# Optimization experiments

Hardware: AMD Instinct MI355X
Metric: run time of the kernel (lower is better)

The kernel has to match this reference:

```python
import jax, jax.numpy as jnp
import numpy as np

HEADS = 8

def setup_inputs() -> dict:
    key = jax.random.key(0)
    k1, k2 = jax.random.split(key)
    f_s = jax.random.normal(k1, (8, 256, 32, 32), dtype=jnp.float32)
    f_t = jax.random.normal(k2, (8, 256, 32, 32), dtype=jnp.float32)
    return {"f_s": f_s, "f_t": f_t}

def _to_tokens(x, heads):
    # 'b (h d) x y -> b h (x y) d'
    b, c, h, w = x.shape
    d = c // heads
    return x.reshape(b, heads, d, h * w).transpose(0, 1, 3, 2)

def reference(f_s, f_t):
    b, c, h, w = f_s.shape
    q = _to_tokens(f_s, HEADS)   # [b, H, n, d]
    k = _to_tokens(f_t, HEADS)
    v = _to_tokens(f_s, HEADS)
    # unscaled QK^T softmax V (faithful to source: no 1/sqrt(d) scaling)
    sim = jnp.einsum('bhid,bhjd->bhij', q, k)          # [b, H, n, n]
    attn = jax.nn.softmax(sim, axis=-1)
    out = jnp.einsum('bhij,bhjd->bhid', attn, v)       # [b, H, n, d]
    # 'b h (x y) d -> b (h d) x y'
    out = out.transpose(0, 1, 3, 2).reshape(b, c, h, w)
    loss = jnp.mean((out - f_t) ** 2)
    return loss
```

## Files before the change

kernel.cpp:

```cpp
#include <hip/hip_runtime.h>
#include <hip/hip_bf16.h>


typedef __attribute__((ext_vector_type(4))) float f32x4;
typedef __attribute__((ext_vector_type(8))) short bf16x8;
typedef __attribute__((ext_vector_type(4))) unsigned u32x4;

#define QOFF 0
#define KOFF 16384
#define VOFF 24576
#define ROFF 32768

__device__ __forceinline__ unsigned cvtpk(float a, float b) {
    unsigned r;
    asm("v_cvt_pk_bf16_f32 %0, %1, %2" : "=v"(r) : "v"(a), "v"(b));
    return r;
}
#define SWAP32(a, b) asm("v_permlane32_swap_b32 %0, %1" : "+v"(a), "+v"(b))
#define SWAP16(a, b) asm("v_permlane16_swap_b32 %0, %1" : "+v"(a), "+v"(b))

__device__ __forceinline__ float exp2fast(float x) {
#if __has_builtin(__builtin_amdgcn_exp2f)
    return __builtin_amdgcn_exp2f(x);
#else
    return exp2f(x);
#endif
}

__global__ __launch_bounds__(512, 2)
void attn_mse_kernel(const float* __restrict__ fs, const float* __restrict__ ft,
                     float* __restrict__ out)
{
    __shared__ __align__(16) unsigned char smem[32832];

    const int tid  = threadIdx.x;
    const int lane = tid & 63;
    const int w    = tid >> 6;
    const int g    = lane >> 4;
    const int c    = lane & 15;

    const int bid  = blockIdx.x;
    const int x    = bid & 7, y = bid >> 3;
    const int pair = x * 8 + (y & 7);
    const int q0   = (y >> 3) * 256;

    const float* qb = fs + (size_t)pair * 32768;
    const float* kb = ft + (size_t)pair * 32768;

    {
        unsigned* lq = (unsigned*)(smem + QOFF) + w * 512;
        #pragma unroll
        for (int is = 0; is < 2; ++is) {
            const int row0 = q0 + w * 32 + is * 16;
            #pragma unroll
            for (int p = 0; p < 4; ++p) {
                const int dp = 4 * p + g;
                const float* src = qb + (size_t)(2 * dp) * 1024 + row0 + c;
                lq[is * 256 + p * 64 + c * 4 + g] =
                    cvtpk(src[0] * 1.44269504f, src[1024] * 1.44269504f);
            }
        }
    }
    const bf16x8 qf0 = *(const bf16x8*)(smem + QOFF + w * 2048 + lane * 16);
    const bf16x8 qf1 = *(const bf16x8*)(smem + QOFF + w * 2048 + 1024 + lane * 16);

    const int s_k = w >> 1, h_k = w & 1;
    float  kr[4];
    float4 vr;
    const int d_v = w * 4 + g;

    auto LOADK = [&](int t) {
        const int row0 = t * 64 + s_k * 16;
        #pragma unroll
        for (int pp = 0; pp < 2; ++pp) {
            const int dp = 4 * (2 * h_k + pp) + g;
            const float* src = kb + (size_t)(2 * dp) * 1024 + row0 + c;
            kr[2 * pp] = src[0]; kr[2 * pp + 1] = src[1024];
        }
    };
    auto LOADV = [&](int t) {
        vr = *(const float4*)(qb + (size_t)d_v * 1024 + t * 64 + 4 * c);
    };
    auto STORE = [&](int buf) {
        unsigned* lk = (unsigned*)(smem + KOFF + buf * 4096) + s_k * 256;
        #pragma unroll
        for (int pp = 0; pp < 2; ++pp) {
            const int p = 2 * h_k + pp;
            lk[p * 64 + c * 4 + g] = cvtpk(kr[2 * pp], kr[2 * pp + 1]);
        }
        unsigned char* lv = smem + VOFF + buf * 4096;
        const unsigned lo = cvtpk(vr.x, vr.y), hi = cvtpk(vr.z, vr.w);
        *(unsigned long long*)(lv + d_v * 128 + ((8 * c) ^ ((d_v & 7) << 4))) =
            (unsigned long long)lo | ((unsigned long long)hi << 32);
    };

    LOADK(0); LOADV(0);
    STORE(0);

    f32x4 O[2][2];
    #pragma unroll
    for (int a = 0; a < 2; ++a)
        #pragma unroll
        for (int b = 0; b < 2; ++b)
            O[a][b] = f32x4{0.f, 0.f, 0.f, 0.f};
    float l0 = 0.f, l1 = 0.f;

    int cur = 0;
    for (int t = 0; t < 16; ++t) {
        if (t < 15) { LOADK(t + 1); LOADV(t + 1); }
        __syncthreads();
        const unsigned char* bK = smem + KOFF + cur * 4096;
        const unsigned char* bV = smem + VOFF + cur * 4096;

        bf16x8 kf[4], vb[2][2];
        #pragma unroll
        for (int Mt = 0; Mt < 4; ++Mt)
            kf[Mt] = *(const bf16x8*)(bK + Mt * 1024 + lane * 16);
        #pragma unroll
        for (int ks = 0; ks < 2; ++ks)
            #pragma unroll
            for (int df = 0; df < 2; ++df)
                vb[ks][df] = *(const bf16x8*)(bV + (c + 16 * df) * 128 +
                               (((unsigned)(ks * 64 + g * 16)) ^ ((c & 7) << 4)));

        f32x4 S[4][2];
        #pragma unroll
        for (int Mt = 0; Mt < 4; ++Mt) {
            const f32x4 z = {0.f, 0.f, 0.f, 0.f};
            S[Mt][0] = __builtin_amdgcn_mfma_f32_16x16x32_bf16(kf[Mt], qf0, z, 0, 0, 0);
            S[Mt][1] = __builtin_amdgcn_mfma_f32_16x16x32_bf16(kf[Mt], qf1, z, 0, 0, 0);
        }

        float ps0 = 0.f, ps1 = 0.f;
        #pragma unroll
        for (int Mt = 0; Mt < 4; ++Mt)
            #pragma unroll
            for (int r = 0; r < 4; ++r) {
                const float p0 = exp2fast(S[Mt][0][r]);
                const float p1 = exp2fast(S[Mt][1][r]);
                S[Mt][0][r] = p0; ps0 += p0;
                S[Mt][1][r] = p1; ps1 += p1;
            }
        l0 += ps0; l1 += ps1;

        #pragma unroll
        for (int is = 0; is < 2; ++is) {
            #pragma unroll
            for (int ks = 0; ks < 2; ++ks) {
                unsigned u0 = cvtpk(S[2 * ks][is][0],     S[2 * ks][is][1]);
                unsigned u1 = cvtpk(S[2 * ks][is][2],     S[2 * ks][is][3]);
                unsigned u2 = cvtpk(S[2 * ks + 1][is][0], S[2 * ks + 1][is][1]);
                unsigned u3 = cvtpk(S[2 * ks + 1][is][2], S[2 * ks + 1][is][3]);
                SWAP32(u0, u2); SWAP32(u1, u3);
                SWAP16(u0, u2); SWAP16(u1, u3);
                const u32x4 pw = {u0, u1, u2, u3};
                const bf16x8 pa = __builtin_bit_cast(bf16x8, pw);
                O[is][0] = __builtin_amdgcn_mfma_f32_16x16x32_bf16(pa, vb[ks][0], O[is][0], 0, 0, 0);
                O[is][1] = __builtin_amdgcn_mfma_f32_16x16x32_bf16(pa, vb[ks][1], O[is][1], 0, 0, 0);
            }
        }

        if (t < 15) STORE(cur ^ 1);
        cur ^= 1;
    }

    l0 += __shfl_xor(l0, 16); l0 += __shfl_xor(l0, 32);
    l1 += __shfl_xor(l1, 16); l1 += __shfl_xor(l1, 32);
    const float li0 = 1.0f / l0;
    const float li1 = 1.0f / l1;

    float acc = 0.f;
    const int n0 = q0 + w * 32;
    #pragma unroll
    for (int is = 0; is < 2; ++is) {
        const float liv = is ? li1 : li0;
        #pragma unroll
        for (int r = 0; r < 4; ++r) {
            const float lr = __shfl(liv, g * 4 + r);
            const int n = n0 + is * 16 + g * 4 + r;
            #pragma unroll
            for (int Nd = 0; Nd < 2; ++Nd) {
                const int d = Nd * 16 + c;
                const float oo = O[is][Nd][r] * lr;
                const float tv = kb[(size_t)d * 1024 + n];
                const float e = oo - tv;
                acc += e * e;
            }
        }
    }
    #pragma unroll
    for (int off = 1; off < 64; off <<= 1) acc += __shfl_xor(acc, off);
    float* lred = (float*)(smem + ROFF);
    if (lane == 0) lred[w] = acc;
    __syncthreads();
    if (tid == 0) {
        float s = 0.f;
        #pragma unroll
        for (int i = 0; i < 8; ++i) s += lred[i];
        atomicAdd(out, s * (1.0f / 2097152.0f));
    }
}

extern "C" void kernel_launch(void* const* d_in, const int* in_sizes, int n_in,
                              void* d_out, int out_size, void* d_ws, size_t ws_size,
                              hipStream_t stream) {
    const float* fs = (const float*)d_in[0];
    const float* ft = (const float*)d_in[1];
    float* out = (float*)d_out;
    hipMemsetAsync(out, 0, sizeof(float), stream);
    attn_mse_kernel<<<dim3(256), dim3(512), 0, stream>>>(fs, ft, out);
}
```

Baseline: 28.46 us.

## Stage full K/V into 128KB LDS upfront, drop per-tile syncs, stagger tile order

Replaces the double-buffered K/V streaming loop with a single upfront load of all 16 K and V tiles into 128KB of shared memory, so the main loop has no barriers. Global loads become float4-vectorised with an XOR-swizzled LDS layout for the K and Q fragments, and each wave starts at a different tile offset to spread LDS bank traffic. MFMA sections are wrapped in s_setprio to favour matrix issue. The cost is losing overlap between global loads and compute, and with 128KB LDS per block only one block fits per CU, which defeats the launch bound of two blocks.

```diff
diff --git a/kernel.cpp b/kernel.cpp
--- a/kernel.cpp
+++ b/kernel.cpp
@@ -6,10 +6,8 @@
 typedef __attribute__((ext_vector_type(8))) short bf16x8;
 typedef __attribute__((ext_vector_type(4))) unsigned u32x4;
 
-#define QOFF 0
-#define KOFF 16384
-#define VOFF 24576
-#define ROFF 32768
+#define KOFF 0
+#define VOFF 65536
 
 __device__ __forceinline__ unsigned cvtpk(float a, float b) {
     unsigned r;
@@ -31,7 +29,7 @@
 void attn_mse_kernel(const float* __restrict__ fs, const float* __restrict__ ft,
                      float* __restrict__ out)
 {
-    __shared__ __align__(16) unsigned char smem[32832];
+    __shared__ __align__(16) unsigned char smem[131072];
 
     const int tid  = threadIdx.x;
     const int lane = tid & 63;
@@ -40,62 +38,60 @@
     const int c    = lane & 15;
 
     const int bid  = blockIdx.x;
-    const int x    = bid & 7, y = bid >> 3;
-    const int pair = x * 8 + (y & 7);
-    const int q0   = (y >> 3) * 256;
+    const int pair = (bid & 7) * 8 + ((bid >> 3) & 7);
+    const int q0   = (bid >> 6) * 256;
 
     const float* qb = fs + (size_t)pair * 32768;
     const float* kb = ft + (size_t)pair * 32768;
 
+    const int p_ = c >> 2, jq = c & 3;
+    const int dp = 4 * p_ + g;
+    const int w0 = p_ * 64 + 16 * jq + 4 * (0 ^ p_) + g;
+    const int w1 = p_ * 64 + 16 * jq + 4 * (1 ^ p_) + g;
+    const int w2 = p_ * 64 + 16 * jq + 4 * (2 ^ p_) + g;
+    const int w3 = p_ * 64 + 16 * jq + 4 * (3 ^ p_) + g;
+
     {
-        unsigned* lq = (unsigned*)(smem + QOFF) + w * 512;
-        #pragma unroll
-        for (int is = 0; is < 2; ++is) {
-            const int row0 = q0 + w * 32 + is * 16;
-            #pragma unroll
-            for (int p = 0; p < 4; ++p) {
-                const int dp = 4 * p + g;
-                const float* src = qb + (size_t)(2 * dp) * 1024 + row0 + c;
-                lq[is * 256 + p * 64 + c * 4 + g] =
-                    cvtpk(src[0] * 1.44269504f, src[1024] * 1.44269504f);
-            }
-        }
-    }
-    const bf16x8 qf0 = *(const bf16x8*)(smem + QOFF + w * 2048 + lane * 16);
-    const bf16x8 qf1 = *(const bf16x8*)(smem + QOFF + w * 2048 + 1024 + lane * 16);
-
-    const int s_k = w >> 1, h_k = w & 1;
-    float  kr[4];
-    float4 vr;
-    const int d_v = w * 4 + g;
-
-    auto LOADK = [&](int t) {
-        const int row0 = t * 64 + s_k * 16;
-        #pragma unroll
-        for (int pp = 0; pp < 2; ++pp) {
-            const int dp = 4 * (2 * h_k + pp) + g;
-            const float* src = kb + (size_t)(2 * dp) * 1024 + row0 + c;
-            kr[2 * pp] = src[0]; kr[2 * pp + 1] = src[1024];
-        }
-    };
-    auto LOADV = [&](int t) {
-        vr = *(const float4*)(qb + (size_t)d_v * 1024 + t * 64 + 4 * c);
-    };
-    auto STORE = [&](int buf) {
-        unsigned* lk = (unsigned*)(smem + KOFF + buf * 4096) + s_k * 256;
-        #pragma unroll
-        for (int pp = 0; pp < 2; ++pp) {
-            const int p = 2 * h_k + pp;
-            lk[p * 64 + c * 4 + g] = cvtpk(kr[2 * pp], kr[2 * pp + 1]);
-        }
-        unsigned char* lv = smem + VOFF + buf * 4096;
-        const unsigned lo = cvtpk(vr.x, vr.y), hi = cvtpk(vr.z, vr.w);
-        *(unsigned long long*)(lv + d_v * 128 + ((8 * c) ^ ((d_v & 7) << 4))) =
-            (unsigned long long)lo | ((unsigned long long)hi << 32);
-    };
-
-    LOADK(0); LOADV(0);
-    STORE(0);
+        const float sc = 1.44269504f;
+        #pragma unroll
+        for (int st = 0; st < 2; ++st) {
+            const float* r0 = qb + (size_t)(2 * dp) * 1024 + (q0 + w * 32 + st * 16) + 4 * jq;
+            const float4 a = *(const float4*)(r0);
+            const float4 b = *(const float4*)(r0 + 1024);
+            unsigned* dst = (unsigned*)(smem + VOFF + w * 2048 + st * 1024);
+            dst[w0] = cvtpk(a.x * sc, b.x * sc);
+            dst[w1] = cvtpk(a.y * sc, b.y * sc);
+            dst[w2] = cvtpk(a.z * sc, b.z * sc);
+            dst[w3] = cvtpk(a.w * sc, b.w * sc);
+        }
+    }
+    const bf16x8 qf0 = *(const bf16x8*)(smem + VOFF + w * 2048 + ((lane ^ g) << 4));
+    const bf16x8 qf1 = *(const bf16x8*)(smem + VOFF + w * 2048 + 1024 + ((lane ^ g) << 4));
+    __syncthreads();
+
+    #pragma unroll
+    for (int st = 0; st < 8; ++st) {
+        const float* r0 = kb + (size_t)(2 * dp) * 1024 + (w * 128 + st * 16) + 4 * jq;
+        const float4 a = *(const float4*)(r0);
+        const float4 b = *(const float4*)(r0 + 1024);
+        unsigned* dst = (unsigned*)(smem + KOFF + (w * 8 + st) * 1024);
+        dst[w0] = cvtpk(a.x, b.x);
+        dst[w1] = cvtpk(a.y, b.y);
+        dst[w2] = cvtpk(a.z, b.z);
+        dst[w3] = cvtpk(a.w, b.w);
+    }
+    {
+        const int dv = w * 4 + g;
+        #pragma unroll
+        for (int tt = 0; tt < 16; ++tt) {
+            const float4 vv = *(const float4*)(qb + (size_t)dv * 1024 + tt * 64 + 4 * c);
+            const unsigned lo = cvtpk(vv.x, vv.y), hi = cvtpk(vv.z, vv.w);
+            *(unsigned long long*)(smem + VOFF + tt * 4096 + dv * 128 +
+                                   ((8 * c) ^ ((dv & 7) << 4))) =
+                (unsigned long long)lo | ((unsigned long long)hi << 32);
+        }
+    }
+    __syncthreads();
 
     f32x4 O[2][2];
     #pragma unroll
@@ -105,17 +101,15 @@
             O[a][b] = f32x4{0.f, 0.f, 0.f, 0.f};
     float l0 = 0.f, l1 = 0.f;
 
-    int cur = 0;
     for (int t = 0; t < 16; ++t) {
-        if (t < 15) { LOADK(t + 1); LOADV(t + 1); }
-        __syncthreads();
-        const unsigned char* bK = smem + KOFF + cur * 4096;
-        const unsigned char* bV = smem + VOFF + cur * 4096;
+        const int tabs = (t + 2 * w) & 15;
+        const unsigned char* bK = smem + KOFF + tabs * 4096;
+        const unsigned char* bV = smem + VOFF + tabs * 4096;
 
         bf16x8 kf[4], vb[2][2];
         #pragma unroll
         for (int Mt = 0; Mt < 4; ++Mt)
-            kf[Mt] = *(const bf16x8*)(bK + Mt * 1024 + lane * 16);
+            kf[Mt] = *(const bf16x8*)(bK + Mt * 1024 + ((lane ^ g) << 4));
         #pragma unroll
         for (int ks = 0; ks < 2; ++ks)
             #pragma unroll
@@ -124,22 +118,24 @@
                                (((unsigned)(ks * 64 + g * 16)) ^ ((c & 7) << 4)));
 
         f32x4 S[4][2];
+        __builtin_amdgcn_s_setprio(1);
         #pragma unroll
         for (int Mt = 0; Mt < 4; ++Mt) {
             const f32x4 z = {0.f, 0.f, 0.f, 0.f};
             S[Mt][0] = __builtin_amdgcn_mfma_f32_16x16x32_bf16(kf[Mt], qf0, z, 0, 0, 0);
             S[Mt][1] = __builtin_amdgcn_mfma_f32_16x16x32_bf16(kf[Mt], qf1, z, 0, 0, 0);
         }
+        __builtin_amdgcn_s_setprio(0);
 
         float ps0 = 0.f, ps1 = 0.f;
         #pragma unroll
         for (int Mt = 0; Mt < 4; ++Mt)
             #pragma unroll
             for (int r = 0; r < 4; ++r) {
-                const float p0 = exp2fast(S[Mt][0][r]);
-                const float p1 = exp2fast(S[Mt][1][r]);
-                S[Mt][0][r] = p0; ps0 += p0;
-                S[Mt][1][r] = p1; ps1 += p1;
+                const float pv0 = exp2fast(S[Mt][0][r]);
+                const float pv1 = exp2fast(S[Mt][1][r]);
+                S[Mt][0][r] = pv0; ps0 += pv0;
+                S[Mt][1][r] = pv1; ps1 += pv1;
             }
         l0 += ps0; l1 += ps1;
 
@@ -155,13 +151,12 @@
                 SWAP16(u0, u2); SWAP16(u1, u3);
                 const u32x4 pw = {u0, u1, u2, u3};
                 const bf16x8 pa = __builtin_bit_cast(bf16x8, pw);
+                __builtin_amdgcn_s_setprio(1);
                 O[is][0] = __builtin_amdgcn_mfma_f32_16x16x32_bf16(pa, vb[ks][0], O[is][0], 0, 0, 0);
                 O[is][1] = __builtin_amdgcn_mfma_f32_16x16x32_bf16(pa, vb[ks][1], O[is][1], 0, 0, 0);
+                __builtin_amdgcn_s_setprio(0);
             }
         }
-
-        if (t < 15) STORE(cur ^ 1);
-        cur ^= 1;
     }
 
     l0 += __shfl_xor(l0, 16); l0 += __shfl_xor(l0, 32);
@@ -190,7 +185,8 @@
     }
     #pragma unroll
     for (int off = 1; off < 64; off <<= 1) acc += __shfl_xor(acc, off);
-    float* lred = (float*)(smem + ROFF);
+    __syncthreads();
+    float* lred = (float*)(smem);
     if (lane == 0) lred[w] = acc;
     __syncthreads();
     if (tid == 0) {
```

Result: no change. 28.02 us (-1.5%).
